# Kernel tuning notes

Measured on AMD Instinct MI355X. Metric: run time of the kernel, lower is better.

Reference implementation:

```python
import jax, jax.numpy as jnp
import numpy as np

H = 128  # hidden_size

def _band_agg(h):
    # Equivalent to bmm(adj, h) with adj = degree-normalized tridiagonal
    # (self + left + right neighbor), degree=3 interior, 2 at endpoints,
    # normalization adj/(deg+1e-8) as in the torch module.
    B, S, D = h.shape
    hp = jnp.pad(h, ((0, 0), (1, 1), (0, 0)))
    s = hp[:, :-2] + hp[:, 1:-1] + hp[:, 2:]            # [B,S,D] neighbor sum
    deg = jnp.full((S,), 3.0, dtype=h.dtype).at[0].set(2.0).at[S - 1].set(2.0)
    return s / (deg + 1e-8)[None, :, None]


def setup_inputs() -> dict:
    key = jax.random.key(0)
    ks = jax.random.split(key, 16)
    f32 = jnp.float32
    p = lambda k, shp: (jax.random.normal(k, shp, dtype=f32) * 0.05)
    return {
        "x": jax.random.normal(ks[0], (32, 2048, 6), dtype=f32),
        "enc_w1": p(ks[1], (6, H)),   "enc_b1": p(ks[2], (H,)),
        "enc_w2": p(ks[3], (H, H)),   "enc_b2": p(ks[4], (H,)),
        "gc1_w": p(ks[5], (H, H)),    "gc1_b": p(ks[6], (H,)),
        "gc2_w": p(ks[7], (H, H)),    "gc2_b": p(ks[8], (H,)),
        "gc3_w": p(ks[9], (H, H)),    "gc3_b": p(ks[10], (H,)),
        "cls_w1": p(ks[11], (H, H // 2)), "cls_b1": p(ks[12], (H // 2,)),
        "cls_w2": p(ks[13], (H // 2, 3)), "cls_b2": p(ks[14], (3,)),
    }


def reference(x, enc_w1, enc_b1, enc_w2, enc_b2,
              gc1_w, gc1_b, gc2_w, gc2_b, gc3_w, gc3_b,
              cls_w1, cls_b1, cls_w2, cls_b2):
    # node encoder: Linear -> ReLU -> Linear
    h = jax.nn.relu(x @ enc_w1 + enc_b1) @ enc_w2 + enc_b2
    # three graph convolutions: linear, normalized tridiagonal aggregate, relu
    h = jax.nn.relu(_band_agg(h @ gc1_w + gc1_b))
    h = jax.nn.relu(_band_agg(h @ gc2_w + gc2_b))
    h = jax.nn.relu(_band_agg(h @ gc3_w + gc3_b))
    # AdaptiveAvgPool1d(1) over seq dim after transpose == mean over nodes
    pooled = h.mean(axis=1)                              # [B, H]
    # classifier (dropout inactive in eval)
    return jax.nn.relu(pooled @ cls_w1 + cls_b1) @ cls_w2 + cls_b2
```

## Files before the change

kernel.cpp:

```cpp
#include <hip/hip_runtime.h>

#define SEQ  2048
#define HID  128
#define NB   32
#define TILE 58
#define GX   36
#define MSTR 67
#define SLOT(m) ((m) + 1)

typedef float f2    __attribute__((ext_vector_type(2)));
typedef float f32x4 __attribute__((ext_vector_type(4)));
typedef short bf16x8 __attribute__((ext_vector_type(8)));
typedef unsigned u32x4 __attribute__((ext_vector_type(4)));

__device__ __forceinline__ void split_bf16(float v, short& h, short& l) {
  unsigned u = __float_as_uint(v);
  unsigned r = (u + 0x7fffu + ((u >> 16) & 1u)) >> 16;
  h = (short)r;
  const float hf = __uint_as_float(r << 16);
  const float lo = v - hf;
  unsigned u2 = __float_as_uint(lo);
  unsigned r2 = (u2 + 0x7fffu + ((u2 >> 16) & 1u)) >> 16;
  l = (short)r2;
}

__device__ __forceinline__ unsigned cvt_pk_bf16(float a, float b) {
  unsigned r;
  asm("v_cvt_pk_bf16_f32 %0, %1, %2" : "=v"(r) : "v"(a), "v"(b));
  return r;
}

__global__ __launch_bounds__(256) void prep_kernel(
    const float* __restrict__ enc_w2, const float* __restrict__ enc_b2,
    const float* __restrict__ gc1_w, const float* __restrict__ gc1_b,
    const float* __restrict__ gc2_w, const float* __restrict__ gc3_w,
    short* __restrict__ Wf, float* __restrict__ bp, unsigned* __restrict__ cnt)
{
  const int tid = threadIdx.x;
  const int bid = blockIdx.x;

  if (bid == 96) {
    if (tid < 128) {
      float s = gc1_b[tid];
      for (int k = 0; k < 128; ++k) s = fmaf(enc_b2[k], gc1_w[k * 128 + tid], s);
      bp[tid] = s;
    }
    if (tid < NB) cnt[tid] = 0u;
    return;
  }

  const int L = bid >> 5, bx = bid & 31;
  short* hi = Wf + L * 32768;
  short* lo = hi + 16384;

  if (L == 0) {
    __shared__ float As[32 * 128];
    __shared__ float Bs[128 * 16];
    const int k0 = (bx >> 3) * 32, n0 = (bx & 7) * 16;
    for (int i = tid; i < 1024; i += 256)
      ((f32x4*)As)[i] = ((const f32x4*)(enc_w2 + k0 * 128))[i];
    for (int i = tid; i < 512; i += 256) {
      const int t = i >> 2, q = i & 3;
      ((f32x4*)Bs)[i] = *(const f32x4*)(gc1_w + t * 128 + n0 + q * 4);
    }
    __syncthreads();
    #pragma unroll
    for (int e = 0; e < 2; ++e) {
      const int f = tid + e * 256;
      const int l = f >> 3, j = f & 7;
      const float* ar = As + ((l >> 4) * 8 + j) * 128;
      const int nn = l & 15;
      float s0 = 0.f, s1 = 0.f, s2 = 0.f, s3 = 0.f;
      for (int t = 0; t < 128; t += 4) {
        s0 = fmaf(ar[t + 0], Bs[(t + 0) * 16 + nn], s0);
        s1 = fmaf(ar[t + 1], Bs[(t + 1) * 16 + nn], s1);
        s2 = fmaf(ar[t + 2], Bs[(t + 2) * 16 + nn], s2);
        s3 = fmaf(ar[t + 3], Bs[(t + 3) * 16 + nn], s3);
      }
      short h, lw;
      split_bf16((s0 + s1) + (s2 + s3), h, lw);
      hi[bx * 512 + f] = h; lo[bx * 512 + f] = lw;
    }
  } else {
    const float* __restrict__ SW = (L == 1) ? gc2_w : gc3_w;
    const int ks = bx >> 3, nt = bx & 7;
    for (int f = tid; f < 512; f += 256) {
      const int l = f >> 3, j = f & 7;
      const int k = ks * 32 + (l >> 4) * 8 + j;
      const int n = nt * 16 + (l & 15);
      short h, lw;
      split_bf16(SW[k * 128 + n], h, lw);
      hi[bx * 512 + f] = h; lo[bx * 512 + f] = lw;
    }
  }
}

__global__ __launch_bounds__(256) void fused_kernel(
    const float* __restrict__ x,
    const float* __restrict__ enc_w1, const float* __restrict__ enc_b1,
    const short* __restrict__ Wf, const float* __restrict__ bp,
    const float* __restrict__ gc2_b, const float* __restrict__ gc3_b,
    float* __restrict__ partial, unsigned* __restrict__ cnt,
    const float* __restrict__ cls_w1, const float* __restrict__ cls_b1,
    const float* __restrict__ cls_w2, const float* __restrict__ cls_b2,
    float* __restrict__ out)
{
  __shared__ float hT[HID * MSTR];
  __shared__ float wsmall[7 * HID];
  __shared__ float psum[256];
  __shared__ int lastf;

  const int tid  = threadIdx.x;
  const int lane = tid & 63;
  const int w    = tid >> 6;
  const int gxb  = blockIdx.x, b = blockIdx.y;
  const int s0   = gxb * TILE;
  const bf16x8* Bf = (const bf16x8*)Wf;

  for (int f = tid; f < 7 * HID; f += 256)
    wsmall[f] = (f < 6 * HID) ? enc_w1[f] : enc_b1[f - 6 * HID];

  const int sm = s0 - 3 + lane;
  float xv[6];
  if (sm >= 0 && sm < SEQ) {
    const f2* xp = (const f2*)(x + ((long long)b * SEQ + sm) * 6);
    const f2 a0 = xp[0], a1 = xp[1], a2 = xp[2];
    xv[0] = a0.x; xv[1] = a0.y; xv[2] = a1.x;
    xv[3] = a1.y; xv[4] = a2.x; xv[5] = a2.y;
  } else {
    #pragma unroll
    for (int k = 0; k < 6; ++k) xv[k] = 0.f;
  }
  __syncthreads();
  {
    const int c0 = w * 32;
    float4 a4[8];
    #pragma unroll
    for (int q = 0; q < 8; ++q) a4[q] = make_float4(0.f, 0.f, 0.f, 0.f);
    #pragma unroll
    for (int k = 0; k < 6; ++k) {
      #pragma unroll
      for (int q = 0; q < 8; ++q) {
        const float4 wv = *(const float4*)&wsmall[k * HID + c0 + q * 4];
        a4[q].x = fmaf(xv[k], wv.x, a4[q].x);
        a4[q].y = fmaf(xv[k], wv.y, a4[q].y);
        a4[q].z = fmaf(xv[k], wv.z, a4[q].z);
        a4[q].w = fmaf(xv[k], wv.w, a4[q].w);
      }
    }
    #pragma unroll
    for (int q = 0; q < 8; ++q) {
      const float4 bb = *(const float4*)&wsmall[6 * HID + c0 + q * 4];
      const int c = c0 + q * 4;
      hT[(c + 0) * MSTR + SLOT(lane)] = fmaxf(a4[q].x + bb.x, 0.f);
      hT[(c + 1) * MSTR + SLOT(lane)] = fmaxf(a4[q].y + bb.y, 0.f);
      hT[(c + 2) * MSTR + SLOT(lane)] = fmaxf(a4[q].z + bb.z, 0.f);
      hT[(c + 3) * MSTR + SLOT(lane)] = fmaxf(a4[q].w + bb.w, 0.f);
    }
  }
  if (tid < 128) {
    hT[tid * MSTR + 0]  = 0.f;
    hT[tid * MSTR + 65] = 0.f;
  }
  __syncthreads();

  const int mt   = w * 16 + (lane & 15);
  const int koct = (lane >> 4) * 8;
  const int stt  = s0 - 3 + mt;
  const float invdA = (stt == 0 || stt == SEQ - 1) ? (1.0f / (2.0f + 1e-8f))
                                                   : (1.0f / (3.0f + 1e-8f));

  #pragma unroll 1
  for (int L = 0; L < 3; ++L) {
    const bf16x8* BhL = Bf + L * 4096;
    const bf16x8* BlL = BhL + 2048;
    const float* bias = (L == 0) ? bp : (L == 1) ? gc2_b : gc3_b;

    f32x4 acc_[8];
    #pragma unroll
    for (int nt = 0; nt < 8; ++nt) acc_[nt] = (f32x4){0.f, 0.f, 0.f, 0.f};

    #pragma unroll 1
    for (int ks = 0; ks < 4; ++ks) {
      const int fb = ks * 512 + lane;
      bf16x8 bh[8], bl[8];
      #pragma unroll
      for (int nt = 0; nt < 8; ++nt) {
        bh[nt] = BhL[fb + nt * 64];
        bl[nt] = BlL[fb + nt * 64];
      }
      bf16x8 ah, al;
      {
        const float* pa = &hT[(ks * 32 + koct) * MSTR + mt];
        float v[8];
        #pragma unroll
        for (int j = 0; j < 8; ++j) {
          if (L == 0) {
            v[j] = pa[j * MSTR + 1];
          } else {
            const float t = (pa[j * MSTR] + pa[j * MSTR + 1] +
                             pa[j * MSTR + 2]) * invdA;
            v[j] = fmaxf(t, 0.f);
          }
        }
        u32x4 hv, lv;
        #pragma unroll
        for (int q = 0; q < 4; ++q) {
          const unsigned hp = cvt_pk_bf16(v[2 * q], v[2 * q + 1]);
          const float h0 = __uint_as_float(hp << 16);
          const float h1 = __uint_as_float(hp & 0xffff0000u);
          hv[q] = hp;
          lv[q] = cvt_pk_bf16(v[2 * q] - h0, v[2 * q + 1] - h1);
        }
        ah = __builtin_bit_cast(bf16x8, hv);
        al = __builtin_bit_cast(bf16x8, lv);
      }
      #pragma unroll
      for (int nt = 0; nt < 8; ++nt) {
        acc_[nt] = __builtin_amdgcn_mfma_f32_16x16x32_bf16(ah, bh[nt], acc_[nt], 0, 0, 0);
        acc_[nt] = __builtin_amdgcn_mfma_f32_16x16x32_bf16(ah, bl[nt], acc_[nt], 0, 0, 0);
        acc_[nt] = __builtin_amdgcn_mfma_f32_16x16x32_bf16(al, bh[nt], acc_[nt], 0, 0, 0);
      }
    }
    __syncthreads();

    {
      const int n0 = lane & 15;
      const int mrow0 = w * 16 + (lane >> 4) * 4;
      #pragma unroll
      for (int nt = 0; nt < 8; ++nt) {
        const float bn = bias[nt * 16 + n0];
        float* pw = &hT[(nt * 16 + n0) * MSTR];
        #pragma unroll
        for (int r = 0; r < 4; ++r) {
          const int m = mrow0 + r;
          const int s = s0 - 3 + m;
          const bool vld = (s >= 0 && s < SEQ);
          pw[SLOT(m)] = vld ? (acc_[nt][r] + bn) : 0.f;
        }
      }
    }
    __syncthreads();
  }

  {
    const int c = tid & 127, half = tid >> 7;
    float ps = 0.f;
    const float* pc = &hT[c * MSTR];
    #pragma unroll 1
    for (int r = 0; r < 29; ++r) {
      const int m = 3 + half * 29 + r;
      const int s = s0 + half * 29 + r;
      if (s < SEQ) {
        const float invd = (s == 0 || s == SEQ - 1) ? (1.0f / (2.0f + 1e-8f))
                                                    : (1.0f / (3.0f + 1e-8f));
        ps += fmaxf((pc[m] + pc[m + 1] + pc[m + 2]) * invd, 0.f);
      }
    }
    psum[tid] = ps;
  }
  __syncthreads();

  if (tid < 128) {
    __hip_atomic_store(&partial[((long long)b * GX + gxb) * HID + tid],
                       psum[tid] + psum[tid + 128],
                       __ATOMIC_RELAXED, __HIP_MEMORY_SCOPE_AGENT);
  }
  asm volatile("s_waitcnt vmcnt(0)" ::: "memory");
  __syncthreads();
  if (tid == 0) {
    const unsigned old = __hip_atomic_fetch_add(&cnt[b], 1u, __ATOMIC_RELAXED,
                                                __HIP_MEMORY_SCOPE_AGENT);
    lastf = (old == GX - 1) ? 1 : 0;
  }
  __syncthreads();
  if (!lastf) return;

  if (tid < 128) {
    float a = 0.f;
    #pragma unroll
    for (int g = 0; g < GX; ++g)
      a += __hip_atomic_load(&partial[((long long)b * GX + g) * HID + tid],
                             __ATOMIC_RELAXED, __HIP_MEMORY_SCOPE_AGENT);
    psum[tid] = a * (1.0f / 2048.0f);
  }
  __syncthreads();
  if (tid < 64) {
    float h = cls_b1[tid];
    for (int k = 0; k < 128; ++k) h = fmaf(psum[k], cls_w1[k * 64 + tid], h);
    psum[128 + tid] = fmaxf(h, 0.f);
  }
  __syncthreads();
  if (tid < 3) {
    float o = cls_b2[tid];
    for (int k = 0; k < 64; ++k) o = fmaf(psum[128 + k], cls_w2[k * 3 + tid], o);
    out[b * 3 + tid] = o;
  }
}

extern "C" void kernel_launch(void* const* d_in, const int* in_sizes, int n_in,
                              void* d_out, int out_size, void* d_ws, size_t ws_size,
                              hipStream_t stream) {
  (void)in_sizes; (void)n_in; (void)out_size; (void)ws_size;
  const float* x      = (const float*)d_in[0];
  const float* enc_w1 = (const float*)d_in[1];
  const float* enc_b1 = (const float*)d_in[2];
  const float* enc_w2 = (const float*)d_in[3];
  const float* enc_b2 = (const float*)d_in[4];
  const float* gc1_w  = (const float*)d_in[5];
  const float* gc1_b  = (const float*)d_in[6];
  const float* gc2_w  = (const float*)d_in[7];
  const float* gc2_b  = (const float*)d_in[8];
  const float* gc3_w  = (const float*)d_in[9];
  const float* gc3_b  = (const float*)d_in[10];
  const float* cls_w1 = (const float*)d_in[11];
  const float* cls_b1 = (const float*)d_in[12];
  const float* cls_w2 = (const float*)d_in[13];
  const float* cls_b2 = (const float*)d_in[14];

  float* bpv     = (float*)d_ws;
  short* Wfrag   = (short*)(bpv + 128);
  float* partial = (float*)(Wfrag + 3 * 2 * 16384);
  unsigned* cntb = (unsigned*)(partial + (long long)NB * GX * HID);

  prep_kernel<<<dim3(97), 256, 0, stream>>>(enc_w2, enc_b2, gc1_w, gc1_b,
                                            gc2_w, gc3_w, Wfrag, bpv, cntb);
  fused_kernel<<<dim3(GX, NB), 256, 0, stream>>>(
      x, enc_w1, enc_b1, Wfrag, bpv, gc2_b, gc3_b, partial, cntb,
      cls_w1, cls_b1, cls_w2, cls_b2, (float*)d_out);
}
```

Baseline: 139.0 us.

## Store activations as bf16 in LDS and drop low-part activation MFMA

After: 170.3 us. +22.5%, slower.

```diff
diff --git a/kernel.cpp b/kernel.cpp
--- a/kernel.cpp
+++ b/kernel.cpp
@@ -28,6 +28,10 @@
   unsigned r;
   asm("v_cvt_pk_bf16_f32 %0, %1, %2" : "=v"(r) : "v"(a), "v"(b));
   return r;
+}
+
+__device__ __forceinline__ float bf2f(short s) {
+  return __uint_as_float(((unsigned)(unsigned short)s) << 16);
 }
 
 __global__ __launch_bounds__(256) void prep_kernel(
@@ -95,7 +99,7 @@
   }
 }
 
-__global__ __launch_bounds__(256) void fused_kernel(
+__global__ __launch_bounds__(256, 5) void fused_kernel(
     const float* __restrict__ x,
     const float* __restrict__ enc_w1, const float* __restrict__ enc_b1,
     const short* __restrict__ Wf, const float* __restrict__ bp,
@@ -105,7 +109,7 @@
     const float* __restrict__ cls_w2, const float* __restrict__ cls_b2,
     float* __restrict__ out)
 {
-  __shared__ float hT[HID * MSTR];
+  __shared__ short hTs[HID * MSTR];
   __shared__ float wsmall[7 * HID];
   __shared__ float psum[256];
   __shared__ int lastf;
@@ -152,15 +156,19 @@
     for (int q = 0; q < 8; ++q) {
       const float4 bb = *(const float4*)&wsmall[6 * HID + c0 + q * 4];
       const int c = c0 + q * 4;
-      hT[(c + 0) * MSTR + SLOT(lane)] = fmaxf(a4[q].x + bb.x, 0.f);
-      hT[(c + 1) * MSTR + SLOT(lane)] = fmaxf(a4[q].y + bb.y, 0.f);
-      hT[(c + 2) * MSTR + SLOT(lane)] = fmaxf(a4[q].z + bb.z, 0.f);
-      hT[(c + 3) * MSTR + SLOT(lane)] = fmaxf(a4[q].w + bb.w, 0.f);
+      const unsigned p01 = cvt_pk_bf16(fmaxf(a4[q].x + bb.x, 0.f),
+                                       fmaxf(a4[q].y + bb.y, 0.f));
+      const unsigned p23 = cvt_pk_bf16(fmaxf(a4[q].z + bb.z, 0.f),
+                                       fmaxf(a4[q].w + bb.w, 0.f));
+      hTs[(c + 0) * MSTR + SLOT(lane)] = (short)(p01 & 0xffffu);
+      hTs[(c + 1) * MSTR + SLOT(lane)] = (short)(p01 >> 16);
+      hTs[(c + 2) * MSTR + SLOT(lane)] = (short)(p23 & 0xffffu);
+      hTs[(c + 3) * MSTR + SLOT(lane)] = (short)(p23 >> 16);
     }
   }
   if (tid < 128) {
-    hT[tid * MSTR + 0]  = 0.f;
-    hT[tid * MSTR + 65] = 0.f;
+    hTs[tid * MSTR + 0]  = 0;
+    hTs[tid * MSTR + 65] = 0;
   }
   __syncthreads();
 
@@ -183,43 +191,47 @@
     #pragma unroll 1
     for (int ks = 0; ks < 4; ++ks) {
       const int fb = ks * 512 + lane;
-      bf16x8 bh[8], bl[8];
-      #pragma unroll
-      for (int nt = 0; nt < 8; ++nt) {
-        bh[nt] = BhL[fb + nt * 64];
-        bl[nt] = BlL[fb + nt * 64];
-      }
-      bf16x8 ah, al;
+      bf16x8 bh[4], bl[4];
+      #pragma unroll
+      for (int i = 0; i < 4; ++i) {
+        bh[i] = BhL[fb + i * 64];
+        bl[i] = BlL[fb + i * 64];
+      }
+      bf16x8 ah;
       {
-        const float* pa = &hT[(ks * 32 + koct) * MSTR + mt];
-        float v[8];
-        #pragma unroll
-        for (int j = 0; j < 8; ++j) {
-          if (L == 0) {
-            v[j] = pa[j * MSTR + 1];
-          } else {
-            const float t = (pa[j * MSTR] + pa[j * MSTR + 1] +
-                             pa[j * MSTR + 2]) * invdA;
+        const short* pa = &hTs[(ks * 32 + koct) * MSTR + mt];
+        if (L == 0) {
+          #pragma unroll
+          for (int j = 0; j < 8; ++j) ah[j] = pa[j * MSTR + 1];
+        } else {
+          float v[8];
+          #pragma unroll
+          for (int j = 0; j < 8; ++j) {
+            const float t = (bf2f(pa[j * MSTR]) + bf2f(pa[j * MSTR + 1]) +
+                             bf2f(pa[j * MSTR + 2])) * invdA;
             v[j] = fmaxf(t, 0.f);
           }
+          u32x4 hv;
+          #pragma unroll
+          for (int q = 0; q < 4; ++q) hv[q] = cvt_pk_bf16(v[2 * q], v[2 * q + 1]);
+          ah = __builtin_bit_cast(bf16x8, hv);
         }
-        u32x4 hv, lv;
-        #pragma unroll
-        for (int q = 0; q < 4; ++q) {
-          const unsigned hp = cvt_pk_bf16(v[2 * q], v[2 * q + 1]);
-          const float h0 = __uint_as_float(hp << 16);
-          const float h1 = __uint_as_float(hp & 0xffff0000u);
-          hv[q] = hp;
-          lv[q] = cvt_pk_bf16(v[2 * q] - h0, v[2 * q + 1] - h1);
-        }
-        ah = __builtin_bit_cast(bf16x8, hv);
-        al = __builtin_bit_cast(bf16x8, lv);
-      }
-      #pragma unroll
-      for (int nt = 0; nt < 8; ++nt) {
-        acc_[nt] = __builtin_amdgcn_mfma_f32_16x16x32_bf16(ah, bh[nt], acc_[nt], 0, 0, 0);
-        acc_[nt] = __builtin_amdgcn_mfma_f32_16x16x32_bf16(ah, bl[nt], acc_[nt], 0, 0, 0);
-        acc_[nt] = __builtin_amdgcn_mfma_f32_16x16x32_bf16(al, bh[nt], acc_[nt], 0, 0, 0);
+      }
+      #pragma unroll
+      for (int i = 0; i < 4; ++i) {
+        acc_[i] = __builtin_amdgcn_mfma_f32_16x16x32_bf16(ah, bh[i], acc_[i], 0, 0, 0);
+        acc_[i] = __builtin_amdgcn_mfma_f32_16x16x32_bf16(ah, bl[i], acc_[i], 0, 0, 0);
+      }
+      __builtin_amdgcn_sched_barrier(0);
+      #pragma unroll
+      for (int i = 0; i < 4; ++i) {
+        bh[i] = BhL[fb + (i + 4) * 64];
+        bl[i] = BlL[fb + (i + 4) * 64];
+      }
+      #pragma unroll
+      for (int i = 0; i < 4; ++i) {
+        acc_[i + 4] = __builtin_amdgcn_mfma_f32_16x16x32_bf16(ah, bh[i], acc_[i + 4], 0, 0, 0);
+        acc_[i + 4] = __builtin_amdgcn_mfma_f32_16x16x32_bf16(ah, bl[i], acc_[i + 4], 0, 0, 0);
       }
     }
     __syncthreads();
@@ -230,14 +242,19 @@
       #pragma unroll
       for (int nt = 0; nt < 8; ++nt) {
         const float bn = bias[nt * 16 + n0];
-        float* pw = &hT[(nt * 16 + n0) * MSTR];
+        short* pw = &hTs[(nt * 16 + n0) * MSTR];
+        float vv[4];
         #pragma unroll
         for (int r = 0; r < 4; ++r) {
-          const int m = mrow0 + r;
-          const int s = s0 - 3 + m;
-          const bool vld = (s >= 0 && s < SEQ);
-          pw[SLOT(m)] = vld ? (acc_[nt][r] + bn) : 0.f;
+          const int s = s0 - 3 + mrow0 + r;
+          vv[r] = (s >= 0 && s < SEQ) ? (acc_[nt][r] + bn) : 0.f;
         }
+        const unsigned p01 = cvt_pk_bf16(vv[0], vv[1]);
+        const unsigned p23 = cvt_pk_bf16(vv[2], vv[3]);
+        pw[SLOT(mrow0) + 0] = (short)(p01 & 0xffffu);
+        pw[SLOT(mrow0) + 1] = (short)(p01 >> 16);
+        pw[SLOT(mrow0) + 2] = (short)(p23 & 0xffffu);
+        pw[SLOT(mrow0) + 3] = (short)(p23 >> 16);
       }
     }
     __syncthreads();
@@ -246,7 +263,7 @@
   {
     const int c = tid & 127, half = tid >> 7;
     float ps = 0.f;
-    const float* pc = &hT[c * MSTR];
+    const short* pc = &hTs[c * MSTR];
     #pragma unroll 1
     for (int r = 0; r < 29; ++r) {
       const int m = 3 + half * 29 + r;
@@ -254,7 +271,7 @@
       if (s < SEQ) {
         const float invd = (s == 0 || s == SEQ - 1) ? (1.0f / (2.0f + 1e-8f))
                                                     : (1.0f / (3.0f + 1e-8f));
-        ps += fmaxf((pc[m] + pc[m + 1] + pc[m + 2]) * invd, 0.f);
+        ps += fmaxf((bf2f(pc[m]) + bf2f(pc[m + 1]) + bf2f(pc[m + 2])) * invd, 0.f);
       }
     }
     psum[tid] = ps;
```
